# Performance work log

Measured on AMD Instinct MI355X. Metric: run time of the kernel, lower is better.

The kernel has to match this reference:

```python
import jax, jax.numpy as jnp
import numpy as np

B, T, E, STRIDE = 32, 4096, 256, 16


def setup_inputs() -> dict:
    key = jax.random.key(0)
    nn_outs = jax.random.normal(key, (B, T, E), dtype=jnp.float32)
    # cut marker (==1) every STRIDE tokens, last position of each segment
    batch_x = jnp.zeros((B, T), dtype=jnp.int64).at[:, STRIDE - 1::STRIDE].set(1)
    return {"nn_outs": nn_outs, "batch_x": batch_x}


def reference(nn_outs, batch_x):
    """Hierarchical pooling: mean-pool nn_outs over segments delimited by
    batch_x == 1. Segment k of a row spans (cut_{k-1}, cut_k] inclusive of the
    cut token; tokens after the last cut are dropped (as in the original).
    Returns (pooled (B, maxlen, E), n_segments (B,))."""
    b, t, e = nn_outs.shape
    is_cut = (batch_x == 1)
    n_cuts = jnp.sum(is_cut, axis=1)                      # (B,) segments per row
    # exclusive cumsum: segment id of token t = #cuts strictly before t
    seg = jnp.cumsum(is_cut, axis=1) - is_cut.astype(jnp.int64)  # (B, T)
    valid = seg < n_cuts[:, None]                         # tokens after last cut dropped
    maxlen = int(jnp.max(n_cuts))                         # padded interm_step
    # flatten to global segment ids; invalid tokens go to a dump bucket
    gseg = jnp.where(valid, seg + jnp.arange(b, dtype=jnp.int64)[:, None] * maxlen,
                     b * maxlen)
    gseg = gseg.reshape(-1)
    flat = nn_outs.reshape(b * t, e)
    n_seg_total = b * maxlen + 1
    sums = jax.ops.segment_sum(flat, gseg, num_segments=n_seg_total)[:-1]
    counts = jax.ops.segment_sum(valid.reshape(-1).astype(nn_outs.dtype), gseg,
                                 num_segments=n_seg_total)[:-1]
    pooled = sums / jnp.maximum(counts, 1)[:, None]       # empty pad segments -> 0
    return pooled.reshape(b, maxlen, e), n_cuts
```

## Files before the change

kernel.cpp:

```cpp
#include <hip/hip_runtime.h>

#define NROWS 32
#define TLEN  4096
#define EDIM  256
#define PER   (TLEN / 256)
#define SEGS_PER_BLOCK 4

__global__ __launch_bounds__(256, 8) void fused_pool_kernel(
    const float* __restrict__ nn,
    const int*  __restrict__ batch_x,
    int maxlen, int nb_per_row,
    float* __restrict__ out,
    float* __restrict__ n_cuts_out)
{
    const int tid  = threadIdx.x;
    const int lane = tid & 63;
    const int w    = tid >> 6;
    const int blk  = blockIdx.x;
    const int b    = blk / nb_per_row;
    const int k0   = (blk - b * nb_per_row) * SEGS_PER_BLOCK;

    __shared__ int s_cuts[TLEN];
    __shared__ int s_wsum[4];

    const int* row = batch_x + (long long)b * TLEN;
    const int t0 = tid * PER;

    unsigned mask = 0;
#pragma unroll
    for (int j = 0; j < PER; j += 4) {
        const int4 v = *(const int4*)(row + t0 + j);
        mask |= (unsigned)(v.x == 1) << (j + 0);
        mask |= (unsigned)(v.y == 1) << (j + 1);
        mask |= (unsigned)(v.z == 1) << (j + 2);
        mask |= (unsigned)(v.w == 1) << (j + 3);
    }
    const int local = __popc(mask);

    int incl = local;
#pragma unroll
    for (int d = 1; d < 64; d <<= 1) {
        const int v = __shfl_up(incl, d, 64);
        if (lane >= d) incl += v;
    }
    if (lane == 63) s_wsum[w] = incl;
    __syncthreads();
    const int s0 = s_wsum[0], s1 = s_wsum[1], s2 = s_wsum[2], s3 = s_wsum[3];
    const int wbase = (w > 0 ? s0 : 0) + (w > 1 ? s1 : 0) + (w > 2 ? s2 : 0);
    const int ncuts = s0 + s1 + s2 + s3;

    int idx = wbase + incl - local;
    unsigned m = mask;
    while (m) {
        const int j = __ffs(m) - 1;
        m &= m - 1;
        s_cuts[idx++] = t0 + j;
    }
    __syncthreads();

    if (k0 == 0 && tid == 0) n_cuts_out[b] = (float)ncuts;

    const int k = k0 + w;
    if (k >= maxlen) return;

    float4 acc = make_float4(0.f, 0.f, 0.f, 0.f);
    if (k < ncuts) {
        const int start = (k == 0) ? 0 : (s_cuts[k - 1] + 1);
        const int end   = s_cuts[k];
        const int cnt   = end - start + 1;
        const float* base = nn + ((long long)b * TLEN + start) * EDIM + lane * 4;

        if (cnt == 16) {
            float4 v[8];
#pragma unroll
            for (int t = 0; t < 8; ++t)
                v[t] = *(const float4*)(base + (long long)t * EDIM);
#pragma unroll
            for (int s = 1; s < 8; s <<= 1)
#pragma unroll
                for (int t = 0; t < 8; t += 2 * s) {
                    v[t].x += v[t + s].x; v[t].y += v[t + s].y;
                    v[t].z += v[t + s].z; v[t].w += v[t + s].w;
                }
            const float4 sum0 = v[0];
#pragma unroll
            for (int t = 0; t < 8; ++t)
                v[t] = *(const float4*)(base + (long long)(8 + t) * EDIM);
#pragma unroll
            for (int s = 1; s < 8; s <<= 1)
#pragma unroll
                for (int t = 0; t < 8; t += 2 * s) {
                    v[t].x += v[t + s].x; v[t].y += v[t + s].y;
                    v[t].z += v[t + s].z; v[t].w += v[t + s].w;
                }
            const float inv = 1.0f / 16.0f;
            acc.x = (sum0.x + v[0].x) * inv;
            acc.y = (sum0.y + v[0].y) * inv;
            acc.z = (sum0.z + v[0].z) * inv;
            acc.w = (sum0.w + v[0].w) * inv;
        } else {
            float4 a0 = make_float4(0.f, 0.f, 0.f, 0.f);
            float4 a1 = a0, a2 = a0, a3 = a0;
            int t = 0;
            for (; t + 4 <= cnt; t += 4) {
                const float4 v0 = *(const float4*)(base + (long long)(t + 0) * EDIM);
                const float4 v1 = *(const float4*)(base + (long long)(t + 1) * EDIM);
                const float4 v2 = *(const float4*)(base + (long long)(t + 2) * EDIM);
                const float4 v3 = *(const float4*)(base + (long long)(t + 3) * EDIM);
                a0.x += v0.x; a0.y += v0.y; a0.z += v0.z; a0.w += v0.w;
                a1.x += v1.x; a1.y += v1.y; a1.z += v1.z; a1.w += v1.w;
                a2.x += v2.x; a2.y += v2.y; a2.z += v2.z; a2.w += v2.w;
                a3.x += v3.x; a3.y += v3.y; a3.z += v3.z; a3.w += v3.w;
            }
            for (; t < cnt; ++t) {
                const float4 v = *(const float4*)(base + (long long)t * EDIM);
                a0.x += v.x; a0.y += v.y; a0.z += v.z; a0.w += v.w;
            }
            const float inv = 1.0f / (float)cnt;
            acc.x = ((a0.x + a1.x) + (a2.x + a3.x)) * inv;
            acc.y = ((a0.y + a1.y) + (a2.y + a3.y)) * inv;
            acc.z = ((a0.z + a1.z) + (a2.z + a3.z)) * inv;
            acc.w = ((a0.w + a1.w) + (a2.w + a3.w)) * inv;
        }
    }
    float4* o = (float4*)(out + ((long long)b * maxlen + k) * EDIM) + lane;
    *o = acc;
}

extern "C" void kernel_launch(void* const* d_in, const int* in_sizes, int n_in,
                              void* d_out, int out_size, void* d_ws, size_t ws_size,
                              hipStream_t stream) {
    const float* nn_outs = (const float*)d_in[0];
    const int*   batch_x = (const int*)d_in[1];
    float* out = (float*)d_out;

    const int B = NROWS;
    const int maxlen = (out_size - B) / (B * EDIM);
    float* n_cuts_out = out + (size_t)B * maxlen * EDIM;

    const int nb_per_row = (maxlen + SEGS_PER_BLOCK - 1) / SEGS_PER_BLOCK;
    const int blocks = B * nb_per_row;

    fused_pool_kernel<<<blocks, 256, 0, stream>>>(nn_outs, batch_x,
                                                  maxlen, nb_per_row,
                                                  out, n_cuts_out);
}
```

Before: 191.4 us.

## Split cut-position scan into a per-row kernel and read cuts from workspace

Moves the batch_x prefix scan and cut compaction out of every pooling block into a separate kernel launched once per row, storing cut indices and counts in workspace. The pooling kernel then reads its segment bounds directly from global memory, so it no longer needs the 16KB shared array or block barriers. This removes redundant rescanning of the marker row by every block and relieves LDS pressure on occupancy. In exchange it adds a second launch, a dependency between the two kernels, and small global writes and reads for the cut list. Vector-type arithmetic is also simplified.

```diff
diff --git a/kernel.cpp b/kernel.cpp
--- a/kernel.cpp
+++ b/kernel.cpp
@@ -6,21 +6,19 @@
 #define PER   (TLEN / 256)
 #define SEGS_PER_BLOCK 4
 
-__global__ __launch_bounds__(256, 8) void fused_pool_kernel(
-    const float* __restrict__ nn,
-    const int*  __restrict__ batch_x,
-    int maxlen, int nb_per_row,
-    float* __restrict__ out,
+typedef float f32x4 __attribute__((ext_vector_type(4)));
+
+__global__ __launch_bounds__(256) void scan_kernel(
+    const int* __restrict__ batch_x,
+    int*  __restrict__ ws_n,
+    int*  __restrict__ ws_cuts,
     float* __restrict__ n_cuts_out)
 {
     const int tid  = threadIdx.x;
     const int lane = tid & 63;
     const int w    = tid >> 6;
-    const int blk  = blockIdx.x;
-    const int b    = blk / nb_per_row;
-    const int k0   = (blk - b * nb_per_row) * SEGS_PER_BLOCK;
+    const int b    = blockIdx.x;
 
-    __shared__ int s_cuts[TLEN];
     __shared__ int s_wsum[4];
 
     const int* row = batch_x + (long long)b * TLEN;
@@ -50,81 +48,79 @@
     const int ncuts = s0 + s1 + s2 + s3;
 
     int idx = wbase + incl - local;
+    int* cuts = ws_cuts + b * TLEN;
     unsigned m = mask;
     while (m) {
         const int j = __ffs(m) - 1;
         m &= m - 1;
-        s_cuts[idx++] = t0 + j;
+        cuts[idx++] = t0 + j;
     }
-    __syncthreads();
+    if (tid == 0) {
+        ws_n[b] = ncuts;
+        n_cuts_out[b] = (float)ncuts;
+    }
+}
 
-    if (k0 == 0 && tid == 0) n_cuts_out[b] = (float)ncuts;
-
-    const int k = k0 + w;
+__global__ __launch_bounds__(256, 8) void pool_kernel(
+    const float* __restrict__ nn,
+    const int*  __restrict__ ws_n,
+    const int*  __restrict__ ws_cuts,
+    int maxlen, int nb_per_row,
+    float* __restrict__ out)
+{
+    const int tid  = threadIdx.x;
+    const int lane = tid & 63;
+    const int w    = tid >> 6;
+    const int blk  = blockIdx.x;
+    const int b    = blk / nb_per_row;
+    const int k    = (blk - b * nb_per_row) * SEGS_PER_BLOCK + w;
     if (k >= maxlen) return;
 
-    float4 acc = make_float4(0.f, 0.f, 0.f, 0.f);
+    f32x4 acc = {0.f, 0.f, 0.f, 0.f};
+    const int ncuts = ws_n[b];
     if (k < ncuts) {
-        const int start = (k == 0) ? 0 : (s_cuts[k - 1] + 1);
-        const int end   = s_cuts[k];
+        const int* cuts = ws_cuts + b * TLEN;
+        const int end   = cuts[k];
+        const int start = (k == 0) ? 0 : (cuts[k - 1] + 1);
         const int cnt   = end - start + 1;
         const float* base = nn + ((long long)b * TLEN + start) * EDIM + lane * 4;
 
         if (cnt == 16) {
-            float4 v[8];
+            f32x4 v[8];
 #pragma unroll
             for (int t = 0; t < 8; ++t)
-                v[t] = *(const float4*)(base + (long long)t * EDIM);
+                v[t] = *(const f32x4*)(base + (long long)t * EDIM);
 #pragma unroll
             for (int s = 1; s < 8; s <<= 1)
 #pragma unroll
-                for (int t = 0; t < 8; t += 2 * s) {
-                    v[t].x += v[t + s].x; v[t].y += v[t + s].y;
-                    v[t].z += v[t + s].z; v[t].w += v[t + s].w;
-                }
-            const float4 sum0 = v[0];
+                for (int t = 0; t < 8; t += 2 * s)
+                    v[t] += v[t + s];
+            const f32x4 sum0 = v[0];
 #pragma unroll
             for (int t = 0; t < 8; ++t)
-                v[t] = *(const float4*)(base + (long long)(8 + t) * EDIM);
+                v[t] = *(const f32x4*)(base + (long long)(8 + t) * EDIM);
 #pragma unroll
             for (int s = 1; s < 8; s <<= 1)
 #pragma unroll
-                for (int t = 0; t < 8; t += 2 * s) {
-                    v[t].x += v[t + s].x; v[t].y += v[t + s].y;
-                    v[t].z += v[t + s].z; v[t].w += v[t + s].w;
-                }
-            const float inv = 1.0f / 16.0f;
-            acc.x = (sum0.x + v[0].x) * inv;
-            acc.y = (sum0.y + v[0].y) * inv;
-            acc.z = (sum0.z + v[0].z) * inv;
-            acc.w = (sum0.w + v[0].w) * inv;
+                for (int t = 0; t < 8; t += 2 * s)
+                    v[t] += v[t + s];
+            acc = (sum0 + v[0]) * (1.0f / 16.0f);
         } else {
-            float4 a0 = make_float4(0.f, 0.f, 0.f, 0.f);
-            float4 a1 = a0, a2 = a0, a3 = a0;
+            f32x4 a0 = {0.f, 0.f, 0.f, 0.f};
+            f32x4 a1 = a0, a2 = a0, a3 = a0;
             int t = 0;
             for (; t + 4 <= cnt; t += 4) {
-                const float4 v0 = *(const float4*)(base + (long long)(t + 0) * EDIM);
-                const float4 v1 = *(const float4*)(base + (long long)(t + 1) * EDIM);
-                const float4 v2 = *(const float4*)(base + (long long)(t + 2) * EDIM);
-                const float4 v3 = *(const float4*)(base + (long long)(t + 3) * EDIM);
-                a0.x += v0.x; a0.y += v0.y; a0.z += v0.z; a0.w += v0.w;
-                a1.x += v1.x; a1.y += v1.y; a1.z += v1.z; a1.w += v1.w;
-                a2.x += v2.x; a2.y += v2.y; a2.z += v2.z; a2.w += v2.w;
-                a3.x += v3.x; a3.y += v3.y; a3.z += v3.z; a3.w += v3.w;
+                a0 += *(const f32x4*)(base + (long long)(t + 0) * EDIM);
+                a1 += *(const f32x4*)(base + (long long)(t + 1) * EDIM);
+                a2 += *(const f32x4*)(base + (long long)(t + 2) * EDIM);
+                a3 += *(const f32x4*)(base + (long long)(t + 3) * EDIM);
             }
-            for (; t < cnt; ++t) {
-                const float4 v = *(const float4*)(base + (long long)t * EDIM);
-                a0.x += v.x; a0.y += v.y; a0.z += v.z; a0.w += v.w;
-            }
-            const float inv = 1.0f / (float)cnt;
-            acc.x = ((a0.x + a1.x) + (a2.x + a3.x)) * inv;
-            acc.y = ((a0.y + a1.y) + (a2.y + a3.y)) * inv;
-            acc.z = ((a0.z + a1.z) + (a2.z + a3.z)) * inv;
-            acc.w = ((a0.w + a1.w) + (a2.w + a3.w)) * inv;
+            for (; t < cnt; ++t)
+                a0 += *(const f32x4*)(base + (long long)t * EDIM);
+            acc = ((a0 + a1) + (a2 + a3)) * (1.0f / (float)cnt);
         }
     }
-    float4* o = (float4*)(out + ((long long)b * maxlen + k) * EDIM) + lane;
-    *o = acc;
+    *((f32x4*)(out + ((long long)b * maxlen + k) * EDIM) + lane) = acc;
 }
 
 extern "C" void kernel_launch(void* const* d_in, const int* in_sizes, int n_in,
@@ -138,10 +134,13 @@
     const int maxlen = (out_size - B) / (B * EDIM);
     float* n_cuts_out = out + (size_t)B * maxlen * EDIM;
 
+    int* ws_n    = (int*)d_ws;
+    int* ws_cuts = ws_n + B;
+
+    scan_kernel<<<B, 256, 0, stream>>>(batch_x, ws_n, ws_cuts, n_cuts_out);
+
     const int nb_per_row = (maxlen + SEGS_PER_BLOCK - 1) / SEGS_PER_BLOCK;
     const int blocks = B * nb_per_row;
-
-    fused_pool_kernel<<<blocks, 256, 0, stream>>>(nn_outs, batch_x,
-                                                  maxlen, nb_per_row,
-                                                  out, n_cuts_out);
+    pool_kernel<<<blocks, 256, 0, stream>>>(nn_outs, ws_n, ws_cuts,
+                                            maxlen, nb_per_row, out);
 }
```

After: 195.3 us. +2.1%, slower.
